# Optimization experiments

Measured on AMD Instinct MI355X. Metric: run time of the kernel, lower is better.

Reference implementation:

```python
import jax, jax.numpy as jnp
import numpy as np
import math

B, H, T, N = 2, 4, 2048, 2048
THETA = 2.0 ** 16


def get_freqs(n: int, theta: float) -> jnp.ndarray:
    # quantize arange to multiples of 2, matching torch (t/2).floor()*2
    t = jnp.arange(n, dtype=jnp.float32)
    q = jnp.floor(t / 2.0) * 2.0
    return 1.0 / theta ** (q / n) / (2.0 * math.pi)


def rope(phases: jnp.ndarray, v: jnp.ndarray) -> jnp.ndarray:
    # v: [B,H,T,N]; phases: [T,N] (broadcast). Interleaved pair rotation.
    ph = (phases % 1.0) * (2.0 * math.pi)
    c, s = jnp.cos(ph), jnp.sin(ph)
    v2 = v.reshape(*v.shape[:-1], -1, 2)           # [...,N/2,2]
    v_rot = jnp.stack((-v2[..., 1], v2[..., 0]), axis=-1).reshape(v.shape)
    return (v * c + v_rot * s).astype(v.dtype)


def setup_inputs() -> dict:
    key = jax.random.key(0)
    kq, kv = jax.random.split(key)
    Q = jax.random.normal(kq, (B, H, T, N), dtype=jnp.float32)
    V = jax.random.normal(kv, (B, H, T, N), dtype=jnp.float32)
    return {"Q": Q, "V": V}


def reference(Q, V):
    Tlen = Q.shape[2]
    n = Q.shape[3]
    freqs = get_freqs(n, THETA)                               # [N]
    phases = jnp.arange(Tlen, dtype=jnp.float32)[:, None] * freqs[None, :]  # [T,N]
    QR = rope(phases, Q)                                      # K is Q -> KR = QR
    scores = jnp.einsum('bhtn,bhsn->bhts', QR, QR)            # [B,H,T,T]
    # strictly-causal mask: keep s < t (tril with diagonal=-1)
    mask = jnp.tril(jnp.ones((Tlen, Tlen), dtype=bool), k=-1)
    scores = jnp.where(mask, scores, 0.0)
    out = jnp.einsum('bhts,bhsn->bhtn', scores, V)
    return out
```

## Files before the change

kernel.cpp:

```cpp
#include <hip/hip_runtime.h>
#include <hip/hip_bf16.h>

#define TDIM 2048
#define NDIM 2048
#define BHN  8
#define LD   2048

typedef __attribute__((ext_vector_type(8))) short bf16x8;
typedef __attribute__((ext_vector_type(4))) float f32x4;
typedef unsigned short us;

static __device__ __forceinline__ us f2bf(float x) {
  union { __hip_bfloat16 h; us u; } cv;
  cv.h = __float2bfloat16(x);
  return cv.u;
}

__global__ __launch_bounds__(256) void rope_kernel(const float* __restrict__ Q,
                                                   us* __restrict__ QR,
                                                   int total8) {
  int idx = blockIdx.x * blockDim.x + threadIdx.x;
  if (idx >= total8) return;
  long base = (long)idx * 8;
  int n = (int)(base & (NDIM - 1));
  int t = (int)((base >> 11) & (TDIM - 1));
  const float4* p = reinterpret_cast<const float4*>(Q + base);
  float4 v0 = p[0], v1 = p[1];
  float q[8] = {v0.x, v0.y, v0.z, v0.w, v1.x, v1.y, v1.z, v1.w};
  us r[8];
  float tf = (float)t;
#pragma unroll
  for (int pr = 0; pr < 4; ++pr) {
    int nn = n + pr * 2;
    float freq = __builtin_exp2f((float)nn * (-1.0f / 128.0f)) * 0.15915494309189535f;
    float ph = tf * freq;
    ph = ph - __builtin_floorf(ph);
    float c = __builtin_amdgcn_cosf(ph);
    float s = __builtin_amdgcn_sinf(ph);
    float e = q[2 * pr], o = q[2 * pr + 1];
    r[2 * pr]     = f2bf(e * c - o * s);
    r[2 * pr + 1] = f2bf(o * c + e * s);
  }
  union { us usv[8]; bf16x8 v; } pk;
#pragma unroll
  for (int i = 0; i < 8; ++i) pk.usv[i] = r[i];
  *reinterpret_cast<bf16x8*>(QR + base) = pk.v;
}

__global__ __launch_bounds__(256) void vtrans_kernel(const float* __restrict__ V,
                                                     us* __restrict__ VT) {
  __shared__ float tile[32][33];
  int bh = blockIdx.z;
  int n0 = blockIdx.x * 32, t0 = blockIdx.y * 32;
  const float* Vp = V + (long)bh * TDIM * NDIM;
  us* Tp = VT + (long)bh * TDIM * NDIM;
  int tx = threadIdx.x, ty = threadIdx.y;
#pragma unroll
  for (int i = 0; i < 4; ++i)
    tile[ty + i * 8][tx] = Vp[(long)(t0 + ty + i * 8) * NDIM + n0 + tx];
  __syncthreads();
#pragma unroll
  for (int i = 0; i < 4; ++i)
    Tp[(long)(n0 + ty + i * 8) * TDIM + t0 + tx] = f2bf(tile[tx][ty + i * 8]);
}

template <int PASS>
__global__ __launch_bounds__(512, 2) void gemm256(
    const us* __restrict__ Abase, const us* __restrict__ Bbase,
    void* __restrict__ Cbase, int nh) {
  extern __shared__ us lds[];
  int bid = (int)blockIdx.x;
  int head, rt = 0, ct, kts = 32, cls = 0;
  if constexpr (PASS == 0) {
    head = bid % nh;
    int tri = bid / nh;
    rt = 0;
    while ((rt + 1) * (rt + 2) / 2 <= tri) ++rt;
    ct = tri - rt * (rt + 1) / 2;
    kts = 32;
  } else {
    head = bid % nh;
    int rem = bid / nh;
    ct = rem & 7;
    cls = rem >> 3;
  }
  const us* A = Abase + (long)head * TDIM * LD;
  const us* B = Bbase + (long)head * TDIM * LD;
  const int tid = (int)threadIdx.x;
  const int lane = tid & 63, wid = tid >> 6;
  const int wr = wid >> 2, wc = wid & 3;
  const int l15 = lane & 15, l4 = lane >> 4;

  f32x4 acc[8][4];
  const int NSEG = (PASS == 0) ? 1 : 2;

#pragma unroll 1
  for (int seg = 0; seg < NSEG; ++seg) {
    if constexpr (PASS == 1) {
      rt = seg ? cls : 7 - cls;
      kts = (rt + 1) * 4;
    }
    const int row0 = rt * 256, col0 = ct * 256;

#pragma unroll
    for (int m = 0; m < 8; ++m)
#pragma unroll
      for (int n = 0; n < 4; ++n) acc[m][n] = (f32x4){0.f, 0.f, 0.f, 0.f};

    auto stage = [&](int half , int t) {
      const us* g0 = (half < 2) ? A : B;
      const int tr0 = (half < 2) ? row0 : col0;
      const int h = half & 1;
      us* lb = lds + ((half < 2) ? 0 : 32768) + (t & 1) * 16384;
      const int k0 = t * 64;
#pragma unroll
      for (int r = 0; r < 2; ++r) {
        int off = r * 512 + tid;
        int row = off >> 3;
        int ch = off & 7;
        int chl = ch ^ (row & 7);
        const us* g = g0 + (long)(tr0 + h * 128 + row) * LD + (k0 + chl * 8);
        us* l = lb + h * 8192 + off * 8;
        __builtin_amdgcn_global_load_lds(
            (const __attribute__((address_space(1))) unsigned int*)g,
            (__attribute__((address_space(3))) unsigned int*)l, 16, 0, 0);
      }
    };
    auto ldA = [&](int b, int m, int ks) -> bf16x8 {
      int row = wr * 128 + m * 16 + l15;
      int ch = (ks * 4 + l4) ^ (row & 7);
      return *reinterpret_cast<const bf16x8*>(lds + b * 16384 + row * 64 + ch * 8);
    };
    auto ldB = [&](int b, int n, int ks) -> bf16x8 {
      int row = wc * 64 + n * 16 + l15;
      int ch = (ks * 4 + l4) ^ (row & 7);
      return *reinterpret_cast<const bf16x8*>(lds + 32768 + b * 16384 + row * 64 + ch * 8);
    };

    stage(0, 0); stage(1, 0); stage(2, 0); stage(3, 0);
    if (1 < kts) { stage(2, 1); stage(3, 1); }
    asm volatile("s_waitcnt vmcnt(4)" ::: "memory");
    __builtin_amdgcn_s_barrier();
    __builtin_amdgcn_sched_barrier(0);

    bf16x8 af[4][2], bfr[4][2];
    for (int t = 0; t < kts; ++t) {
      const int b = t & 1;
#pragma unroll
      for (int m = 0; m < 4; ++m) { af[m][0] = ldA(b, m, 0); af[m][1] = ldA(b, m, 1); }
#pragma unroll
      for (int n = 0; n < 2; ++n) { bfr[n][0] = ldB(b, n, 0); bfr[n][1] = ldB(b, n, 1); }
      if (t + 1 < kts) stage(0, t + 1);
      __builtin_amdgcn_s_barrier();
      asm volatile("s_waitcnt lgkmcnt(0)" ::: "memory");
      __builtin_amdgcn_sched_barrier(0);
      __builtin_amdgcn_s_setprio(1);
#pragma unroll
      for (int m = 0; m < 4; ++m)
#pragma unroll
        for (int n = 0; n < 2; ++n)
#pragma unroll
          for (int ks = 0; ks < 2; ++ks)
            acc[m][n] = __builtin_amdgcn_mfma_f32_16x16x32_bf16(af[m][ks], bfr[n][ks], acc[m][n], 0, 0, 0);
      __builtin_amdgcn_s_setprio(0);
      __builtin_amdgcn_sched_barrier(0);
      __builtin_amdgcn_s_barrier();
#pragma unroll
      for (int n = 2; n < 4; ++n) { bfr[n][0] = ldB(b, n, 0); bfr[n][1] = ldB(b, n, 1); }
      if (t + 1 < kts) stage(1, t + 1);
      __builtin_amdgcn_s_barrier();
      asm volatile("s_waitcnt lgkmcnt(0)" ::: "memory");
      __builtin_amdgcn_sched_barrier(0);
      __builtin_amdgcn_s_setprio(1);
#pragma unroll
      for (int m = 0; m < 4; ++m)
#pragma unroll
        for (int n = 2; n < 4; ++n)
#pragma unroll
          for (int ks = 0; ks < 2; ++ks)
            acc[m][n] = __builtin_amdgcn_mfma_f32_16x16x32_bf16(af[m][ks], bfr[n][ks], acc[m][n], 0, 0, 0);
      __builtin_amdgcn_s_setprio(0);
      __builtin_amdgcn_sched_barrier(0);
      __builtin_amdgcn_s_barrier();
#pragma unroll
      for (int m = 0; m < 4; ++m) { af[m][0] = ldA(b, m + 4, 0); af[m][1] = ldA(b, m + 4, 1); }
      if (t + 2 < kts) stage(2, t + 2);
      __builtin_amdgcn_s_barrier();
      asm volatile("s_waitcnt lgkmcnt(0)" ::: "memory");
      __builtin_amdgcn_sched_barrier(0);
      __builtin_amdgcn_s_setprio(1);
#pragma unroll
      for (int m = 0; m < 4; ++m)
#pragma unroll
        for (int n = 0; n < 2; ++n)
#pragma unroll
          for (int ks = 0; ks < 2; ++ks)
            acc[m + 4][n] = __builtin_amdgcn_mfma_f32_16x16x32_bf16(af[m][ks], bfr[n][ks], acc[m + 4][n], 0, 0, 0);
      __builtin_amdgcn_s_setprio(0);
      __builtin_amdgcn_sched_barrier(0);
      __builtin_amdgcn_s_barrier();
      if (t + 2 < kts) stage(3, t + 2);
      __builtin_amdgcn_s_setprio(1);
#pragma unroll
      for (int m = 0; m < 4; ++m)
#pragma unroll
        for (int n = 2; n < 4; ++n)
#pragma unroll
          for (int ks = 0; ks < 2; ++ks)
            acc[m + 4][n] = __builtin_amdgcn_mfma_f32_16x16x32_bf16(af[m][ks], bfr[n][ks], acc[m + 4][n], 0, 0, 0);
      __builtin_amdgcn_s_setprio(0);
      if (t + 2 < kts) { asm volatile("s_waitcnt vmcnt(4)" ::: "memory"); }
      else             { asm volatile("s_waitcnt vmcnt(0)" ::: "memory"); }
      __builtin_amdgcn_sched_barrier(0);
      __builtin_amdgcn_s_barrier();
      __builtin_amdgcn_sched_barrier(0);
    }

    if constexpr (PASS == 0) {
      us* C = (us*)Cbase + (long)head * TDIM * LD;
      const bool diag = (rt == ct);
#pragma unroll
      for (int m = 0; m < 8; ++m) {
        int r0 = row0 + wr * 128 + m * 16 + l4 * 4;
#pragma unroll
        for (int n = 0; n < 4; ++n) {
          int cc = col0 + wc * 64 + n * 16 + l15;
#pragma unroll
          for (int j = 0; j < 4; ++j) {
            int tt = r0 + j;
            float v = acc[m][n][j];
            if (diag && cc >= tt) v = 0.0f;
            C[(long)tt * LD + cc] = f2bf(v);
          }
        }
      }
    } else {
      float* C = (float*)Cbase + (long)head * TDIM * LD;
#pragma unroll
      for (int m = 0; m < 8; ++m) {
        int r0 = row0 + wr * 128 + m * 16 + l4 * 4;
#pragma unroll
        for (int n = 0; n < 4; ++n) {
          int cc = col0 + wc * 64 + n * 16 + l15;
#pragma unroll
          for (int j = 0; j < 4; ++j)
            C[(long)(r0 + j) * LD + cc] = acc[m][n][j];
        }
      }
    }
  }
}

extern "C" void kernel_launch(void* const* d_in, const int* in_sizes, int n_in,
                              void* d_out, int out_size, void* d_ws, size_t ws_size,
                              hipStream_t stream) {
  const float* Q = (const float*)d_in[0];
  const float* V = (const float*)d_in[1];
  float* Out = (float*)d_out;
  char* ws = (char*)d_ws;
  const long TN = (long)TDIM * NDIM;
  const size_t BUF = (size_t)BHN * TN * 2;
  const size_t PERBH = (size_t)TN * 2;
  const int SHMEM = 131072;

  hipFuncSetAttribute(reinterpret_cast<const void*>(&gemm256<0>),
                      hipFuncAttributeMaxDynamicSharedMemorySize, SHMEM);
  hipFuncSetAttribute(reinterpret_cast<const void*>(&gemm256<1>),
                      hipFuncAttributeMaxDynamicSharedMemorySize, SHMEM);

  if (ws_size >= 3 * BUF) {
    us* QRb = (us*)ws;
    us* VbT = (us*)(ws + BUF);
    us* S   = (us*)(ws + 2 * BUF);
    int total8 = (int)(BHN * TN / 8);
    rope_kernel<<<dim3(total8 / 256), dim3(256), 0, stream>>>(Q, QRb, total8);
    vtrans_kernel<<<dim3(64, 64, 8), dim3(32, 8), 0, stream>>>(V, VbT);
    gemm256<0><<<dim3(36 * BHN), dim3(512), SHMEM, stream>>>(QRb, QRb, S, BHN);
    gemm256<1><<<dim3(32 * BHN), dim3(512), SHMEM, stream>>>(S, VbT, Out, BHN);
  } else {
    us* QR0 = (us*)ws;
    us* VT0 = (us*)(ws + PERBH);
    us* S0  = (us*)(ws + 2 * PERBH);
    int total8 = (int)(TN / 8);
    for (int bh = 0; bh < BHN; ++bh) {
      rope_kernel<<<dim3(total8 / 256), dim3(256), 0, stream>>>(Q + bh * TN, QR0, total8);
      vtrans_kernel<<<dim3(64, 64, 1), dim3(32, 8), 0, stream>>>(V + bh * TN, VT0);
      gemm256<0><<<dim3(36), dim3(512), SHMEM, stream>>>(QR0, QR0, S0, 1);
      gemm256<1><<<dim3(32), dim3(512), SHMEM, stream>>>(S0, VT0, Out + bh * TN, 1);
    }
  }
}
```

Measured before the change: 269.5 us.

## Fuse both attention GEMMs into one cooperative kernel with per-tile readiness flags

```diff
diff --git a/kernel.cpp b/kernel.cpp
--- a/kernel.cpp
+++ b/kernel.cpp
@@ -48,8 +48,17 @@
 }
 
 __global__ __launch_bounds__(256) void vtrans_kernel(const float* __restrict__ V,
-                                                     us* __restrict__ VT) {
+                                                     us* __restrict__ VT,
+                                                     us* __restrict__ Sflag) {
   __shared__ float tile[32][33];
+  if (Sflag != nullptr && blockIdx.x == 0 && blockIdx.y == 0 && blockIdx.z == 0 &&
+      threadIdx.x == 0 && threadIdx.y == 0) {
+    for (int h = 0; h < BHN; ++h) {
+      unsigned* f = (unsigned*)(Sflag + (long)h * TDIM * LD + 1792);
+      for (int i = 0; i < 36; ++i)
+        __hip_atomic_store(&f[i], 0u, __ATOMIC_RELAXED, __HIP_MEMORY_SCOPE_AGENT);
+    }
+  }
   int bh = blockIdx.z;
   int n0 = blockIdx.x * 32, t0 = blockIdx.y * 32;
   const float* Vp = V + (long)bh * TDIM * NDIM;
@@ -62,6 +71,225 @@
 #pragma unroll
   for (int i = 0; i < 4; ++i)
     Tp[(long)(n0 + ty + i * 8) * TDIM + t0 + tx] = f2bf(tile[tx][ty + i * 8]);
+}
+
+template <int PASS>
+__device__ __forceinline__ void run_tile(const us* __restrict__ A,
+                                         const us* __restrict__ B,
+                                         void* __restrict__ Cbase,
+                                         us* __restrict__ lds,
+                                         int rt, int ct, int tid,
+                                         unsigned* __restrict__ fh) {
+  const int lane = tid & 63, wid = tid >> 6;
+  const int wr = wid >> 2, wc = wid & 3;
+  const int l15 = lane & 15, l4 = lane >> 4;
+  const int row0 = rt * 256, col0 = ct * 256;
+  const int kts = (PASS == 0) ? 32 : (rt + 1) * 4;
+  const int fbase = rt * (rt + 1) / 2;
+
+  auto waitflag = [&](int idx) {
+    if (tid == 0) {
+      while (__hip_atomic_fetch_add(&fh[idx], 0u, __ATOMIC_RELAXED,
+                                    __HIP_MEMORY_SCOPE_AGENT) == 0u)
+        __builtin_amdgcn_s_sleep(4);
+    }
+    __builtin_amdgcn_s_barrier();
+  };
+
+  f32x4 acc[8][4];
+#pragma unroll
+  for (int m = 0; m < 8; ++m)
+#pragma unroll
+    for (int n = 0; n < 4; ++n) acc[m][n] = (f32x4){0.f, 0.f, 0.f, 0.f};
+
+  auto stage = [&](int half , int t) {
+    const us* g0 = (half < 2) ? A : B;
+    const int tr0 = (half < 2) ? row0 : col0;
+    const int h = half & 1;
+    us* lb = lds + ((half < 2) ? 0 : 32768) + (t & 1) * 16384;
+    const int k0 = t * 64;
+#pragma unroll
+    for (int r = 0; r < 2; ++r) {
+      int off = r * 512 + tid;
+      int row = off >> 3;
+      int ch = off & 7;
+      int chl = ch ^ (row & 7);
+      const us* g = g0 + (long)(tr0 + h * 128 + row) * LD + (k0 + chl * 8);
+      us* l = lb + h * 8192 + off * 8;
+      __builtin_amdgcn_global_load_lds(
+          (const __attribute__((address_space(1))) unsigned int*)g,
+          (__attribute__((address_space(3))) unsigned int*)l, 16, 0, 0);
+    }
+  };
+  auto ldA = [&](int b, int m, int ks) -> bf16x8 {
+    int row = wr * 128 + m * 16 + l15;
+    int ch = (ks * 4 + l4) ^ (row & 7);
+    return *reinterpret_cast<const bf16x8*>(lds + b * 16384 + row * 64 + ch * 8);
+  };
+  auto ldB = [&](int b, int n, int ks) -> bf16x8 {
+    int row = wc * 64 + n * 16 + l15;
+    int ch = (ks * 4 + l4) ^ (row & 7);
+    return *reinterpret_cast<const bf16x8*>(lds + 32768 + b * 16384 + row * 64 + ch * 8);
+  };
+
+  if constexpr (PASS == 1) waitflag(fbase);
+
+  stage(0, 0); stage(1, 0); stage(2, 0); stage(3, 0);
+  if (1 < kts) { stage(2, 1); stage(3, 1); }
+  asm volatile("s_waitcnt vmcnt(4)" ::: "memory");
+  __builtin_amdgcn_s_barrier();
+  __builtin_amdgcn_sched_barrier(0);
+
+  bf16x8 af[4][2], bfr[4][2];
+  for (int t = 0; t < kts; ++t) {
+    const int b = t & 1;
+    if constexpr (PASS == 1) {
+      int tn = t + 1;
+      if (tn < kts && (tn & 3) == 0) waitflag(fbase + (tn >> 2));
+    }
+#pragma unroll
+    for (int m = 0; m < 4; ++m) { af[m][0] = ldA(b, m, 0); af[m][1] = ldA(b, m, 1); }
+#pragma unroll
+    for (int n = 0; n < 2; ++n) { bfr[n][0] = ldB(b, n, 0); bfr[n][1] = ldB(b, n, 1); }
+    if (t + 1 < kts) stage(0, t + 1);
+    __builtin_amdgcn_s_barrier();
+    asm volatile("s_waitcnt lgkmcnt(0)" ::: "memory");
+    __builtin_amdgcn_sched_barrier(0);
+    __builtin_amdgcn_s_setprio(1);
+#pragma unroll
+    for (int m = 0; m < 4; ++m)
+#pragma unroll
+      for (int n = 0; n < 2; ++n)
+#pragma unroll
+        for (int ks = 0; ks < 2; ++ks)
+          acc[m][n] = __builtin_amdgcn_mfma_f32_16x16x32_bf16(af[m][ks], bfr[n][ks], acc[m][n], 0, 0, 0);
+    __builtin_amdgcn_s_setprio(0);
+    __builtin_amdgcn_sched_barrier(0);
+    __builtin_amdgcn_s_barrier();
+#pragma unroll
+    for (int n = 2; n < 4; ++n) { bfr[n][0] = ldB(b, n, 0); bfr[n][1] = ldB(b, n, 1); }
+    if (t + 1 < kts) stage(1, t + 1);
+    __builtin_amdgcn_s_barrier();
+    asm volatile("s_waitcnt lgkmcnt(0)" ::: "memory");
+    __builtin_amdgcn_sched_barrier(0);
+    __builtin_amdgcn_s_setprio(1);
+#pragma unroll
+    for (int m = 0; m < 4; ++m)
+#pragma unroll
+      for (int n = 2; n < 4; ++n)
+#pragma unroll
+        for (int ks = 0; ks < 2; ++ks)
+          acc[m][n] = __builtin_amdgcn_mfma_f32_16x16x32_bf16(af[m][ks], bfr[n][ks], acc[m][n], 0, 0, 0);
+    __builtin_amdgcn_s_setprio(0);
+    __builtin_amdgcn_sched_barrier(0);
+    __builtin_amdgcn_s_barrier();
+#pragma unroll
+    for (int m = 0; m < 4; ++m) { af[m][0] = ldA(b, m + 4, 0); af[m][1] = ldA(b, m + 4, 1); }
+    if (t + 2 < kts) stage(2, t + 2);
+    __builtin_amdgcn_s_barrier();
+    asm volatile("s_waitcnt lgkmcnt(0)" ::: "memory");
+    __builtin_amdgcn_sched_barrier(0);
+    __builtin_amdgcn_s_setprio(1);
+#pragma unroll
+    for (int m = 0; m < 4; ++m)
+#pragma unroll
+      for (int n = 0; n < 2; ++n)
+#pragma unroll
+        for (int ks = 0; ks < 2; ++ks)
+          acc[m + 4][n] = __builtin_amdgcn_mfma_f32_16x16x32_bf16(af[m][ks], bfr[n][ks], acc[m + 4][n], 0, 0, 0);
+    __builtin_amdgcn_s_setprio(0);
+    __builtin_amdgcn_sched_barrier(0);
+    __builtin_amdgcn_s_barrier();
+    if (t + 2 < kts) stage(3, t + 2);
+    __builtin_amdgcn_s_setprio(1);
+#pragma unroll
+    for (int m = 0; m < 4; ++m)
+#pragma unroll
+      for (int n = 2; n < 4; ++n)
+#pragma unroll
+        for (int ks = 0; ks < 2; ++ks)
+          acc[m + 4][n] = __builtin_amdgcn_mfma_f32_16x16x32_bf16(af[m][ks], bfr[n][ks], acc[m + 4][n], 0, 0, 0);
+    __builtin_amdgcn_s_setprio(0);
+    if (t + 2 < kts) { asm volatile("s_waitcnt vmcnt(4)" ::: "memory"); }
+    else             { asm volatile("s_waitcnt vmcnt(0)" ::: "memory"); }
+    __builtin_amdgcn_sched_barrier(0);
+    __builtin_amdgcn_s_barrier();
+    __builtin_amdgcn_sched_barrier(0);
+  }
+
+  if constexpr (PASS == 0) {
+    us* C = (us*)Cbase;
+    const bool diag = (rt == ct);
+#pragma unroll
+    for (int m = 0; m < 8; ++m) {
+      int r0 = row0 + wr * 128 + m * 16 + l4 * 4;
+#pragma unroll
+      for (int n = 0; n < 4; ++n) {
+        int cc = col0 + wc * 64 + n * 16 + l15;
+#pragma unroll
+        for (int j = 0; j < 4; ++j) {
+          int tt = r0 + j;
+          float v = acc[m][n][j];
+          if (diag && cc >= tt) v = 0.0f;
+          C[(long)tt * LD + cc] = f2bf(v);
+        }
+      }
+    }
+    __syncthreads();
+    if (tid == 0)
+      __hip_atomic_store(&fh[fbase + ct], 1u, __ATOMIC_RELEASE,
+                         __HIP_MEMORY_SCOPE_AGENT);
+  } else {
+    float* C = (float*)Cbase;
+#pragma unroll
+    for (int m = 0; m < 8; ++m) {
+      int r0 = row0 + wr * 128 + m * 16 + l4 * 4;
+#pragma unroll
+      for (int n = 0; n < 4; ++n) {
+        int cc = col0 + wc * 64 + n * 16 + l15;
+#pragma unroll
+        for (int j = 0; j < 4; ++j)
+          C[(long)(r0 + j) * LD + cc] = acc[m][n][j];
+      }
+    }
+  }
+}
+
+__global__ __launch_bounds__(512, 2) void gemm_fused(const us* __restrict__ QR,
+                                                     const us* __restrict__ VT,
+                                                     us* __restrict__ S,
+                                                     float* __restrict__ Out) {
+  extern __shared__ us lds[];
+  const int b = (int)blockIdx.x;
+  const int head = b & 7, u = b >> 3;
+  const int tid = (int)threadIdx.x;
+  const us* QRh = QR + (long)head * TDIM * LD;
+  const us* VTh = VT + (long)head * TDIM * LD;
+  us* Sh = S + (long)head * TDIM * LD;
+  float* Oh = Out + (long)head * TDIM * LD;
+  unsigned* fh = (unsigned*)(Sh + 1792);
+
+  const int nt0 = (u < 4) ? 2 : 1;
+#pragma unroll 1
+  for (int i = 0; i < nt0; ++i) {
+    int tri = (i == 0) ? u : 32 + u;
+    int rt = 0;
+    while ((rt + 1) * (rt + 2) / 2 <= tri) ++rt;
+    int ct = tri - rt * (rt + 1) / 2;
+    run_tile<0>(QRh, QRh, Sh, lds, rt, ct, tid, fh);
+  }
+
+  int prt[3], pct[3], np;
+  if (u < 4)       { prt[0] = 1; pct[0] = u; np = 1; }
+  else if (u < 8)  { prt[0] = 1; pct[0] = u; prt[1] = 7; pct[1] = u - 4; np = 2; }
+  else if (u < 12) { prt[0] = 0; pct[0] = 2 * (u - 8); prt[1] = 0; pct[1] = 2 * (u - 8) + 1;
+                     prt[2] = 7; pct[2] = u - 4; np = 3; }
+  else if (u < 20) { prt[0] = 2; pct[0] = u - 12; prt[1] = 6; pct[1] = u - 12; np = 2; }
+  else if (u < 28) { prt[0] = 3; pct[0] = u - 20; prt[1] = 5; pct[1] = u - 20; np = 2; }
+  else             { prt[0] = 4; pct[0] = 2 * (u - 28); prt[1] = 4; pct[1] = 2 * (u - 28) + 1; np = 2; }
+#pragma unroll 1
+  for (int i = 0; i < np; ++i)
+    run_tile<1>(Sh, VTh, Oh, lds, prt[i], pct[i], tid, fh);
 }
 
 template <int PASS>
@@ -70,14 +298,13 @@
     void* __restrict__ Cbase, int nh) {
   extern __shared__ us lds[];
   int bid = (int)blockIdx.x;
-  int head, rt = 0, ct, kts = 32, cls = 0;
+  int head, rt = 0, ct, cls = 0;
   if constexpr (PASS == 0) {
     head = bid % nh;
     int tri = bid / nh;
     rt = 0;
     while ((rt + 1) * (rt + 2) / 2 <= tri) ++rt;
     ct = tri - rt * (rt + 1) / 2;
-    kts = 32;
   } else {
     head = bid % nh;
     int rem = bid / nh;
@@ -86,167 +313,20 @@
   }
   const us* A = Abase + (long)head * TDIM * LD;
   const us* B = Bbase + (long)head * TDIM * LD;
+  us* Sh = (us*)Cbase + (long)head * TDIM * LD;
   const int tid = (int)threadIdx.x;
-  const int lane = tid & 63, wid = tid >> 6;
-  const int wr = wid >> 2, wc = wid & 3;
-  const int l15 = lane & 15, l4 = lane >> 4;
-
-  f32x4 acc[8][4];
   const int NSEG = (PASS == 0) ? 1 : 2;
-
 #pragma unroll 1
   for (int seg = 0; seg < NSEG; ++seg) {
-    if constexpr (PASS == 1) {
-      rt = seg ? cls : 7 - cls;
-      kts = (rt + 1) * 4;
-    }
-    const int row0 = rt * 256, col0 = ct * 256;
-
-#pragma unroll
-    for (int m = 0; m < 8; ++m)
-#pragma unroll
-      for (int n = 0; n < 4; ++n) acc[m][n] = (f32x4){0.f, 0.f, 0.f, 0.f};
-
-    auto stage = [&](int half , int t) {
-      const us* g0 = (half < 2) ? A : B;
-      const int tr0 = (half < 2) ? row0 : col0;
-      const int h = half & 1;
-      us* lb = lds + ((half < 2) ? 0 : 32768) + (t & 1) * 16384;
-      const int k0 = t * 64;
-#pragma unroll
-      for (int r = 0; r < 2; ++r) {
-        int off = r * 512 + tid;
-        int row = off >> 3;
-        int ch = off & 7;
-        int chl = ch ^ (row & 7);
-        const us* g = g0 + (long)(tr0 + h * 128 + row) * LD + (k0 + chl * 8);
-        us* l = lb + h * 8192 + off * 8;
-        __builtin_amdgcn_global_load_lds(
-            (const __attribute__((address_space(1))) unsigned int*)g,
-            (__attribute__((address_space(3))) unsigned int*)l, 16, 0, 0);
-      }
-    };
-    auto ldA = [&](int b, int m, int ks) -> bf16x8 {
-      int row = wr * 128 + m * 16 + l15;
-      int ch = (ks * 4 + l4) ^ (row & 7);
-      return *reinterpret_cast<const bf16x8*>(lds + b * 16384 + row * 64 + ch * 8);
-    };
-    auto ldB = [&](int b, int n, int ks) -> bf16x8 {
-      int row = wc * 64 + n * 16 + l15;
-      int ch = (ks * 4 + l4) ^ (row & 7);
-      return *reinterpret_cast<const bf16x8*>(lds + 32768 + b * 16384 + row * 64 + ch * 8);
-    };
-
-    stage(0, 0); stage(1, 0); stage(2, 0); stage(3, 0);
-    if (1 < kts) { stage(2, 1); stage(3, 1); }
-    asm volatile("s_waitcnt vmcnt(4)" ::: "memory");
-    __builtin_amdgcn_s_barrier();
-    __builtin_amdgcn_sched_barrier(0);
-
-    bf16x8 af[4][2], bfr[4][2];
-    for (int t = 0; t < kts; ++t) {
-      const int b = t & 1;
-#pragma unroll
-      for (int m = 0; m < 4; ++m) { af[m][0] = ldA(b, m, 0); af[m][1] = ldA(b, m, 1); }
-#pragma unroll
-      for (int n = 0; n < 2; ++n) { bfr[n][0] = ldB(b, n, 0); bfr[n][1] = ldB(b, n, 1); }
-      if (t + 1 < kts) stage(0, t + 1);
-      __builtin_amdgcn_s_barrier();
-      asm volatile("s_waitcnt lgkmcnt(0)" ::: "memory");
-      __builtin_amdgcn_sched_barrier(0);
-      __builtin_amdgcn_s_setprio(1);
-#pragma unroll
-      for (int m = 0; m < 4; ++m)
-#pragma unroll
-        for (int n = 0; n < 2; ++n)
-#pragma unroll
-          for (int ks = 0; ks < 2; ++ks)
-            acc[m][n] = __builtin_amdgcn_mfma_f32_16x16x32_bf16(af[m][ks], bfr[n][ks], acc[m][n], 0, 0, 0);
-      __builtin_amdgcn_s_setprio(0);
-      __builtin_amdgcn_sched_barrier(0);
-      __builtin_amdgcn_s_barrier();
-#pragma unroll
-      for (int n = 2; n < 4; ++n) { bfr[n][0] = ldB(b, n, 0); bfr[n][1] = ldB(b, n, 1); }
-      if (t + 1 < kts) stage(1, t + 1);
-      __builtin_amdgcn_s_barrier();
-      asm volatile("s_waitcnt lgkmcnt(0)" ::: "memory");
-      __builtin_amdgcn_sched_barrier(0);
-      __builtin_amdgcn_s_setprio(1);
-#pragma unroll
-      for (int m = 0; m < 4; ++m)
-#pragma unroll
-        for (int n = 2; n < 4; ++n)
-#pragma unroll
-          for (int ks = 0; ks < 2; ++ks)
-            acc[m][n] = __builtin_amdgcn_mfma_f32_16x16x32_bf16(af[m][ks], bfr[n][ks], acc[m][n], 0, 0, 0);
-      __builtin_amdgcn_s_setprio(0);
-      __builtin_amdgcn_sched_barrier(0);
-      __builtin_amdgcn_s_barrier();
-#pragma unroll
-      for (int m = 0; m < 4; ++m) { af[m][0] = ldA(b, m + 4, 0); af[m][1] = ldA(b, m + 4, 1); }
-      if (t + 2 < kts) stage(2, t + 2);
-      __builtin_amdgcn_s_barrier();
-      asm volatile("s_waitcnt lgkmcnt(0)" ::: "memory");
-      __builtin_amdgcn_sched_barrier(0);
-      __builtin_amdgcn_s_setprio(1);
-#pragma unroll
-      for (int m = 0; m < 4; ++m)
-#pragma unroll
-        for (int n = 0; n < 2; ++n)
-#pragma unroll
-          for (int ks = 0; ks < 2; ++ks)
-            acc[m + 4][n] = __builtin_amdgcn_mfma_f32_16x16x32_bf16(af[m][ks], bfr[n][ks], acc[m + 4][n], 0, 0, 0);
-      __builtin_amdgcn_s_setprio(0);
-      __builtin_amdgcn_sched_barrier(0);
-      __builtin_amdgcn_s_barrier();
-      if (t + 2 < kts) stage(3, t + 2);
-      __builtin_amdgcn_s_setprio(1);
-#pragma unroll
-      for (int m = 0; m < 4; ++m)
-#pragma unroll
-        for (int n = 2; n < 4; ++n)
-#pragma unroll
-          for (int ks = 0; ks < 2; ++ks)
-            acc[m + 4][n] = __builtin_amdgcn_mfma_f32_16x16x32_bf16(af[m][ks], bfr[n][ks], acc[m + 4][n], 0, 0, 0);
-      __builtin_amdgcn_s_setprio(0);
-      if (t + 2 < kts) { asm volatile("s_waitcnt vmcnt(4)" ::: "memory"); }
-      else             { asm volatile("s_waitcnt vmcnt(0)" ::: "memory"); }
-      __builtin_amdgcn_sched_barrier(0);
-      __builtin_amdgcn_s_barrier();
-      __builtin_amdgcn_sched_barrier(0);
-    }
-
+    int rts = rt, cts = ct;
+    if constexpr (PASS == 1) { rts = seg ? cls : 7 - cls; cts = ct; }
     if constexpr (PASS == 0) {
-      us* C = (us*)Cbase + (long)head * TDIM * LD;
-      const bool diag = (rt == ct);
-#pragma unroll
-      for (int m = 0; m < 8; ++m) {
-        int r0 = row0 + wr * 128 + m * 16 + l4 * 4;
-#pragma unroll
-        for (int n = 0; n < 4; ++n) {
-          int cc = col0 + wc * 64 + n * 16 + l15;
-#pragma unroll
-          for (int j = 0; j < 4; ++j) {
-            int tt = r0 + j;
-            float v = acc[m][n][j];
-            if (diag && cc >= tt) v = 0.0f;
-            C[(long)tt * LD + cc] = f2bf(v);
-          }
-        }
-      }
+      run_tile<0>(A, A, Sh, lds, rts, cts, tid,
+                  (unsigned*)(Sh + 1792));
     } else {
-      float* C = (float*)Cbase + (long)head * TDIM * LD;
-#pragma unroll
-      for (int m = 0; m < 8; ++m) {
-        int r0 = row0 + wr * 128 + m * 16 + l4 * 4;
-#pragma unroll
-        for (int n = 0; n < 4; ++n) {
-          int cc = col0 + wc * 64 + n * 16 + l15;
-#pragma unroll
-          for (int j = 0; j < 4; ++j)
-            C[(long)(r0 + j) * LD + cc] = acc[m][n][j];
-        }
-      }
+      float* Oh = (float*)Cbase + (long)head * TDIM * LD;
+      run_tile<1>(A, B, Oh, lds, rts, cts, tid,
+                  (unsigned*)((us*)Abase + (long)head * TDIM * LD + 1792));
     }
   }
 }
@@ -263,6 +343,8 @@
   const size_t PERBH = (size_t)TN * 2;
   const int SHMEM = 131072;
 
+  hipFuncSetAttribute(reinterpret_cast<const void*>(&gemm_fused),
+                      hipFuncAttributeMaxDynamicSharedMemorySize, SHMEM);
   hipFuncSetAttribute(reinterpret_cast<const void*>(&gemm256<0>),
                       hipFuncAttributeMaxDynamicSharedMemorySize, SHMEM);
   hipFuncSetAttribute(reinterpret_cast<const void*>(&gemm256<1>),
@@ -274,9 +356,16 @@
     us* S   = (us*)(ws + 2 * BUF);
     int total8 = (int)(BHN * TN / 8);
     rope_kernel<<<dim3(total8 / 256), dim3(256), 0, stream>>>(Q, QRb, total8);
-    vtrans_kernel<<<dim3(64, 64, 8), dim3(32, 8), 0, stream>>>(V, VbT);
-    gemm256<0><<<dim3(36 * BHN), dim3(512), SHMEM, stream>>>(QRb, QRb, S, BHN);
-    gemm256<1><<<dim3(32 * BHN), dim3(512), SHMEM, stream>>>(S, VbT, Out, BHN);
+    vtrans_kernel<<<dim3(64, 64, 8), dim3(32, 8), 0, stream>>>(V, VbT, S);
+    void* args[] = {(void*)&QRb, (void*)&VbT, (void*)&S, (void*)&Out};
+    hipError_t ce = hipLaunchCooperativeKernel(
+        reinterpret_cast<const void*>(&gemm_fused), dim3(256), dim3(512),
+        args, (unsigned)SHMEM, stream);
+    if (ce != hipSuccess) {
+      (void)hipGetLastError();
+      gemm256<0><<<dim3(36 * BHN), dim3(512), SHMEM, stream>>>(QRb, QRb, S, BHN);
+      gemm256<1><<<dim3(32 * BHN), dim3(512), SHMEM, stream>>>(S, VbT, Out, BHN);
+    }
   } else {
     us* QR0 = (us*)ws;
     us* VT0 = (us*)(ws + PERBH);
@@ -284,7 +373,7 @@
     int total8 = (int)(TN / 8);
     for (int bh = 0; bh < BHN; ++bh) {
       rope_kernel<<<dim3(total8 / 256), dim3(256), 0, stream>>>(Q + bh * TN, QR0, total8);
-      vtrans_kernel<<<dim3(64, 64, 1), dim3(32, 8), 0, stream>>>(V + bh * TN, VT0);
+      vtrans_kernel<<<dim3(64, 64, 1), dim3(32, 8), 0, stream>>>(V + bh * TN, VT0, S0);
       gemm256<0><<<dim3(36), dim3(512), SHMEM, stream>>>(QR0, QR0, S0, 1);
       gemm256<1><<<dim3(32), dim3(512), SHMEM, stream>>>(S0, VT0, Out + bh * TN, 1);
     }
```

New measurement: 276.4 us. 1.03x slower.
